# Performance work log

Hardware: AMD Instinct MI355X
Metric: run time of the kernel (lower is better)

## Reference

```python
import jax, jax.numpy as jnp
import numpy as np

B, C, H, W = 8, 256, 64, 64
CQK = C // 8  # 32


def setup_inputs() -> dict:
    key = jax.random.key(0)
    ks = jax.random.split(key, 8)
    s = 0.05
    return {
        "x": jax.random.normal(ks[0], (B, C, H, W), dtype=jnp.float32),
        "wq": jax.random.normal(ks[1], (CQK, C), dtype=jnp.float32) * s,
        "bq": jax.random.normal(ks[2], (CQK,), dtype=jnp.float32) * s,
        "wk": jax.random.normal(ks[3], (CQK, C), dtype=jnp.float32) * s,
        "bk": jax.random.normal(ks[4], (CQK,), dtype=jnp.float32) * s,
        "wv": jax.random.normal(ks[5], (C, C), dtype=jnp.float32) * s,
        "bv": jax.random.normal(ks[6], (C,), dtype=jnp.float32) * s,
        "gamma": jax.random.normal(ks[7], (1,), dtype=jnp.float32),
    }


def reference(x, wq, bq, wk, bk, wv, bv, gamma):
    b, c, h, w = x.shape
    xf = x.reshape(b, c, h * w)  # [B, C, N]
    # conv1d kernel-size-1 == per-token linear over channels
    f = jnp.einsum('oc,bcn->bon', wq, xf) + bq[None, :, None]  # [B, C/8, N]
    g = jnp.einsum('oc,bcn->bon', wk, xf) + bk[None, :, None]  # [B, C/8, N]
    hh = jnp.einsum('oc,bcn->bon', wv, xf) + bv[None, :, None]  # [B, C, N]
    # scores[b, i, j] = sum_o f[b, o, i] * g[b, o, j]; NO 1/sqrt(d) scaling
    scores = jnp.einsum('boi,boj->bij', f, g)  # [B, N, N]
    # softmax over dim=1 (the f/query index axis), as in the original
    beta = jax.nn.softmax(scores, axis=1)
    # o[b, c, j] = gamma * sum_i hh[b, c, i] * beta[b, i, j] + xf
    o = gamma[0] * jnp.einsum('bci,bij->bcj', hh, beta) + xf
    return o.reshape(b, c, h, w)
```

## Files before the change

### kernel.cpp

```cpp
#include <hip/hip_runtime.h>
#include <stdint.h>

#define B_ 8
#define C_ 256
#define N_ 4096
#define LOG2E 1.44269504088896f
#define NSHIFT_L2E (-14.0f * 1.44269504088896f)

typedef _Float16 half8 __attribute__((ext_vector_type(8)));
typedef _Float16 half4 __attribute__((ext_vector_type(4)));
typedef float floatx4 __attribute__((ext_vector_type(4)));

__global__ __launch_bounds__(256) void k_wprep(const float* __restrict__ wq, const float* __restrict__ bq,
                                               const float* __restrict__ wk, const float* __restrict__ bk,
                                               const float* __restrict__ wv, const float* __restrict__ bv,
                                               _Float16* __restrict__ Whf, float* __restrict__ Bh) {
    int r = blockIdx.x;
    int t = threadIdx.x;
    const float* src;
    float bias;
    if (r < 32)      { src = wq + r * 256;        bias = bq[r]; }
    else if (r < 64) { src = wk + (r - 32) * 256; bias = bk[r - 32]; }
    else             { src = wv + (r - 64) * 256; bias = bv[r - 64]; }
    Whf[(t >> 3) * 2560 + r * 8 + (t & 7)] = (_Float16)src[t];
    if (t == 0) Bh[r] = bias;
}

__global__ __launch_bounds__(256) void k_proj(const float* __restrict__ x,
                                              const _Float16* __restrict__ Whf,
                                              const float* __restrict__ Bh,
                                              _Float16* __restrict__ Kf,
                                              _Float16* __restrict__ Qf,
                                              _Float16* __restrict__ Vf) {
    __shared__ float xtile[64 * 65];
    __shared__ _Float16 As[64 * 264] __attribute__((aligned(16)));
    int id = blockIdx.x;
    int b  = id & 7;
    int i0 = (id >> 3) * 64;
    int t = threadIdx.x;
    int w = t >> 6, lane = t & 63, col = lane & 15, q = lane >> 4;
    const float* xb = x + (size_t)b * C_ * N_ + i0;
    for (int cc = 0; cc < 4; ++cc) {
        int cr = t >> 4;
        int ip = (t & 15) * 4;
#pragma unroll
        for (int k = 0; k < 4; ++k)
            *(float4*)&xtile[(cr + 16 * k) * 65 + ip] =
                *(const float4*)&xb[(size_t)(cc * 64 + cr + 16 * k) * N_ + ip];
        __syncthreads();
        int i = t & 63, cb2 = (t >> 6) * 16;
        float v[16];
#pragma unroll
        for (int k = 0; k < 16; ++k) v[k] = xtile[(cb2 + k) * 65 + i];
        half8 h0, h1;
#pragma unroll
        for (int k = 0; k < 8; ++k) { h0[k] = (_Float16)v[k]; h1[k] = (_Float16)v[8 + k]; }
        *(half8*)&As[i * 264 + cc * 64 + cb2] = h0;
        *(half8*)&As[i * 264 + cc * 64 + cb2 + 8] = h1;
        __syncthreads();
    }
    floatx4 acc[4][5];
#pragma unroll
    for (int mt = 0; mt < 4; ++mt)
#pragma unroll
        for (int nt = 0; nt < 5; ++nt) acc[mt][nt] = (floatx4){0.f, 0.f, 0.f, 0.f};
    for (int kc = 0; kc < 8; ++kc) {
        half8 a[4], bf[5];
#pragma unroll
        for (int nt = 0; nt < 5; ++nt)
            bf[nt] = *(const half8*)&Whf[(kc * 4 + q) * 2560 + (w * 80 + nt * 16 + col) * 8];
#pragma unroll
        for (int mt = 0; mt < 4; ++mt)
            a[mt] = *(const half8*)&As[(mt * 16 + col) * 264 + kc * 32 + q * 8];
#pragma unroll
        for (int mt = 0; mt < 4; ++mt)
#pragma unroll
            for (int nt = 0; nt < 5; ++nt)
                acc[mt][nt] = __builtin_amdgcn_mfma_f32_16x16x32_f16(a[mt], bf[nt], acc[mt][nt], 0, 0, 0);
    }
#pragma unroll
    for (int nt = 0; nt < 5; ++nt) {
        int n = w * 80 + nt * 16 + col;
        float bias = Bh[n];
        if (n < 32) {
#pragma unroll
            for (int mt = 0; mt < 4; ++mt)
#pragma unroll
                for (int r = 0; r < 4; ++r) {
                    int i = i0 + mt * 16 + q * 4 + r;
                    Kf[((((size_t)b * 128 + (i >> 5)) * 4 + (n >> 3)) * 32 + (i & 31)) * 8 + (n & 7)]
                        = (_Float16)(acc[mt][nt][r] + bias);
                }
        } else if (n < 64) {
            int n2 = n - 32;
#pragma unroll
            for (int mt = 0; mt < 4; ++mt)
#pragma unroll
                for (int r = 0; r < 4; ++r) {
                    int j = i0 + mt * 16 + q * 4 + r;
                    Qf[((((size_t)b * 128 + (j >> 5)) * 4 + (n2 >> 3)) * 32 + (j & 31)) * 8 + (n2 & 7)]
                        = (_Float16)(acc[mt][nt][r] + bias);
                }
        } else {
            int c = n - 64;
#pragma unroll
            for (int mt = 0; mt < 4; ++mt) {
                int ib = (i0 >> 4) + mt;
                half4 v4;
#pragma unroll
                for (int r = 0; r < 4; ++r) v4[r] = (_Float16)(acc[mt][nt][r] + bias);
                *(half4*)&Vf[(((size_t)b * 256 + ib) * 256 + c) * 16 + q * 4] = v4;
            }
        }
    }
}

#define PS_BUF 4608

#define ATTN_STEP(IT, VCUR, VNXT, ROFF, WOFF)                                     \
    {                                                                             \
        if ((IT) < 63) {                                                          \
            _Pragma("unroll")                                                     \
            for (int ct = 0; ct < 2; ++ct) {                                      \
                VNXT[ct * 2 + 0] = *(const half8*)(pV0 + ct * 256);               \
                VNXT[ct * 2 + 1] = *(const half8*)(pV1 + ct * 256);               \
            }                                                                     \
            pV0 += 16384; pV1 += 16384;                                           \
            aKn0 = *(const half8*)(pK);                                           \
            aKn1 = *(const half8*)(pK + 128);                                     \
            pK += 2048;                                                           \
        }                                                                         \
        _Pragma("unroll")                                                         \
        for (int kk = 0; kk < 2; ++kk) {                                          \
            half8 bfr[4];                                                         \
            _Pragma("unroll")                                                     \
            for (int jt = 0; jt < 4; ++jt)                                        \
                bfr[jt] = *(const half8*)&PsF[psr + (ROFF) + jt * 1152 + kk * 32];\
            _Pragma("unroll")                                                     \
            for (int ct = 0; ct < 2; ++ct)                                        \
                _Pragma("unroll")                                                 \
                for (int jt = 0; jt < 4; ++jt)                                    \
                    acc[ct][jt] = __builtin_amdgcn_mfma_f32_16x16x32_f16(         \
                        VCUR[ct * 2 + kk], bfr[jt], acc[ct][jt], 0, 0, 0);        \
        }                                                                         \
        if ((IT) < 63) {                                                          \
            _Pragma("unroll")                                                     \
            for (int itl = 0; itl < 2; ++itl) {                                   \
                floatx4 s = __builtin_amdgcn_mfma_f32_16x16x32_f16(               \
                    itl ? aKn1 : aKn0, bq, (floatx4){0.f, 0.f, 0.f, 0.f}, 0, 0, 0);\
                float p0 = exp2f(s[0] * LOG2E + NSHIFT_L2E);                      \
                float p1 = exp2f(s[1] * LOG2E + NSHIFT_L2E);                      \
                float p2 = exp2f(s[2] * LOG2E + NSHIFT_L2E);                      \
                float p3 = exp2f(s[3] * LOG2E + NSHIFT_L2E);                      \
                lacc += (p0 + p1) + (p2 + p3);                                    \
                half4 ph;                                                         \
                ph[0] = (_Float16)p0; ph[1] = (_Float16)p1;                       \
                ph[2] = (_Float16)p2; ph[3] = (_Float16)p3;                       \
                *(half4*)&PsF[psw + (WOFF) + itl * 16] = ph;                      \
            }                                                                     \
        }                                                                         \
        __syncthreads();                                                          \
    }

__global__ __launch_bounds__(512, 4) void k_attn(const _Float16* __restrict__ Kf,
                                                 const _Float16* __restrict__ Qf,
                                                 const _Float16* __restrict__ Vf,
                                                 const float* __restrict__ x,
                                                 const float* __restrict__ gptr,
                                                 float* __restrict__ out) {
    __shared__ _Float16 PsF[2 * PS_BUF] __attribute__((aligned(16)));
    __shared__ float Lp[2][64];
    int id = blockIdx.x;
    int b  = id & 7;
    int j0 = (id >> 3) * 64;
    int t = threadIdx.x;
    int w = t >> 6, lane = t & 63, col = lane & 15, q = lane >> 4;
    int jts = w & 3, ihs = w >> 2;
    int cw  = w * 32;
    const _Float16* Kfb = Kf + (size_t)b * 131072;
    const _Float16* Qfb = Qf + (size_t)b * 131072;
    const _Float16* Vfb = Vf + (size_t)b * 1048576;
    const _Float16* pK  = Kfb + ((ihs * 4 + q) * 32 + col) * 8;
    const _Float16* pV0 = Vfb + ((q >> 1) * 256 + cw + col) * 16 + (q & 1) * 8;
    const _Float16* pV1 = pV0 + 8192;
    const int psw = (jts * 16 + col) * 72 + ihs * 32 + q * 4;
    const int psr = col * 72 + q * 8;
    floatx4 acc[2][4];
#pragma unroll
    for (int ct = 0; ct < 2; ++ct)
#pragma unroll
        for (int jt = 0; jt < 4; ++jt) acc[ct][jt] = (floatx4){0.f, 0.f, 0.f, 0.f};
    float lacc = 0.f;
    half8 vA[4], vB[4], aKn0, aKn1;
#pragma unroll
    for (int ct = 0; ct < 2; ++ct) {
        vA[ct * 2 + 0] = *(const half8*)(pV0 + ct * 256);
        vA[ct * 2 + 1] = *(const half8*)(pV1 + ct * 256);
    }
    pV0 += 16384; pV1 += 16384;
    aKn0 = *(const half8*)(pK);
    aKn1 = *(const half8*)(pK + 128);
    pK += 2048;
    int jj = j0 + jts * 16;
    half8 bq = *(const half8*)&Qfb[(((jj >> 5) * 4 + q) * 32 + ((jj & 31) + col)) * 8];
#pragma unroll
    for (int itl = 0; itl < 2; ++itl) {
        floatx4 s = __builtin_amdgcn_mfma_f32_16x16x32_f16(itl ? aKn1 : aKn0, bq,
                                                           (floatx4){0.f, 0.f, 0.f, 0.f}, 0, 0, 0);
        float p0 = exp2f(s[0] * LOG2E + NSHIFT_L2E);
        float p1 = exp2f(s[1] * LOG2E + NSHIFT_L2E);
        float p2 = exp2f(s[2] * LOG2E + NSHIFT_L2E);
        float p3 = exp2f(s[3] * LOG2E + NSHIFT_L2E);
        lacc += (p0 + p1) + (p2 + p3);
        half4 ph;
        ph[0] = (_Float16)p0; ph[1] = (_Float16)p1;
        ph[2] = (_Float16)p2; ph[3] = (_Float16)p3;
        *(half4*)&PsF[psw + itl * 16] = ph;
    }
    __syncthreads();
    for (int m = 0; m < 32; ++m) {
        int it = m * 2;
        ATTN_STEP(it,     vA, vB, 0,      PS_BUF)
        ATTN_STEP(it + 1, vB, vA, PS_BUF, 0)
    }
    lacc += __shfl_xor(lacc, 16, 64);
    lacc += __shfl_xor(lacc, 32, 64);
    if (lane < 16) Lp[ihs][jts * 16 + lane] = lacc;
    __syncthreads();
    float gamma = gptr[0];
    const float* xb = x + (size_t)b * C_ * N_;
    float* ob = out + (size_t)b * C_ * N_;
#pragma unroll
    for (int jt = 0; jt < 4; ++jt) {
        int jl = jt * 16 + col;
        float li = 1.0f / (Lp[0][jl] + Lp[1][jl]);
        int j = j0 + jl;
#pragma unroll
        for (int ct = 0; ct < 2; ++ct)
#pragma unroll
            for (int r = 0; r < 4; ++r) {
                int c = cw + ct * 16 + q * 4 + r;
                size_t off = (size_t)c * N_ + j;
                ob[off] = gamma * acc[ct][jt][r] * li + xb[off];
            }
    }
}

extern "C" void kernel_launch(void* const* d_in, const int* in_sizes, int n_in,
                              void* d_out, int out_size, void* d_ws, size_t ws_size,
                              hipStream_t stream) {
    const float* x  = (const float*)d_in[0];
    const float* wq = (const float*)d_in[1];
    const float* bq = (const float*)d_in[2];
    const float* wk = (const float*)d_in[3];
    const float* bk = (const float*)d_in[4];
    const float* wv = (const float*)d_in[5];
    const float* bv = (const float*)d_in[6];
    const float* gm = (const float*)d_in[7];
    float* out = (float*)d_out;
    char* ws = (char*)d_ws;
    _Float16* Vf  = (_Float16*)ws;
    _Float16* Kf  = (_Float16*)(ws + 16777216);
    _Float16* Qf  = (_Float16*)(ws + 18874368);
    _Float16* Whf = (_Float16*)(ws + 20971520);
    float*    Bh  = (float*)(ws + 21135360);

    k_wprep<<<dim3(320), 256, 0, stream>>>(wq, bq, wk, bk, wv, bv, Whf, Bh);
    k_proj<<<dim3(512), 256, 0, stream>>>(x, Whf, Bh, Kf, Qf, Vf);
    k_attn<<<dim3(512), 512, 0, stream>>>(Kf, Qf, Vf, x, gm, out);
}
```

Baseline: 192.6 us.

## Fold log2e into K projection, swizzle P smem, pack-convert and lighten barrier

The K projection output is pre-scaled by log2e, and the softmax shift is passed as the MFMA accumulator init. This removes a per-element FMA before each exp2. The P tile in shared memory drops its padded stride for an XOR-swizzled layout that avoids bank conflicts, and fp16 conversion uses packed round-toward-zero conversions. __syncthreads is replaced by an explicit lgkmcnt wait plus s_barrier, so outstanding global loads no longer stall the barrier. Round-toward-zero conversion and the fp16 rounding of the prescaled K slightly change numerics.

```diff
diff --git a/kernel.cpp b/kernel.cpp
--- a/kernel.cpp
+++ b/kernel.cpp
@@ -9,6 +9,7 @@
 
 typedef _Float16 half8 __attribute__((ext_vector_type(8)));
 typedef _Float16 half4 __attribute__((ext_vector_type(4)));
+typedef __fp16  fp16x2 __attribute__((ext_vector_type(2)));
 typedef float floatx4 __attribute__((ext_vector_type(4)));
 
 __global__ __launch_bounds__(256) void k_wprep(const float* __restrict__ wq, const float* __restrict__ bq,
@@ -89,7 +90,7 @@
                 for (int r = 0; r < 4; ++r) {
                     int i = i0 + mt * 16 + q * 4 + r;
                     Kf[((((size_t)b * 128 + (i >> 5)) * 4 + (n >> 3)) * 32 + (i & 31)) * 8 + (n & 7)]
-                        = (_Float16)(acc[mt][nt][r] + bias);
+                        = (_Float16)((acc[mt][nt][r] + bias) * LOG2E);
                 }
         } else if (n < 64) {
             int n2 = n - 32;
@@ -115,7 +116,7 @@
     }
 }
 
-#define PS_BUF 4608
+#define PS_BUF 4096
 
 #define ATTN_STEP(IT, VCUR, VNXT, ROFF, WOFF)                                     \
     {                                                                             \
@@ -135,7 +136,7 @@
             half8 bfr[4];                                                         \
             _Pragma("unroll")                                                     \
             for (int jt = 0; jt < 4; ++jt)                                        \
-                bfr[jt] = *(const half8*)&PsF[psr + (ROFF) + jt * 1152 + kk * 32];\
+                bfr[jt] = *(const half8*)&PsF[(ROFF) + jt * 1024 + (kk ? ro1 : ro0)]; \
             _Pragma("unroll")                                                     \
             for (int ct = 0; ct < 2; ++ct)                                        \
                 _Pragma("unroll")                                                 \
@@ -147,19 +148,20 @@
             _Pragma("unroll")                                                     \
             for (int itl = 0; itl < 2; ++itl) {                                   \
                 floatx4 s = __builtin_amdgcn_mfma_f32_16x16x32_f16(               \
-                    itl ? aKn1 : aKn0, bq, (floatx4){0.f, 0.f, 0.f, 0.f}, 0, 0, 0);\
-                float p0 = exp2f(s[0] * LOG2E + NSHIFT_L2E);                      \
-                float p1 = exp2f(s[1] * LOG2E + NSHIFT_L2E);                      \
-                float p2 = exp2f(s[2] * LOG2E + NSHIFT_L2E);                      \
-                float p3 = exp2f(s[3] * LOG2E + NSHIFT_L2E);                      \
+                    itl ? aKn1 : aKn0, bq, cns, 0, 0, 0);                         \
+                float p0 = exp2f(s[0]);                                           \
+                float p1 = exp2f(s[1]);                                           \
+                float p2 = exp2f(s[2]);                                           \
+                float p3 = exp2f(s[3]);                                           \
                 lacc += (p0 + p1) + (p2 + p3);                                    \
-                half4 ph;                                                         \
-                ph[0] = (_Float16)p0; ph[1] = (_Float16)p1;                       \
-                ph[2] = (_Float16)p2; ph[3] = (_Float16)p3;                       \
-                *(half4*)&PsF[psw + (WOFF) + itl * 16] = ph;                      \
+                union { fp16x2 v; uint32_t u; } plo, phi;                         \
+                plo.v = __builtin_amdgcn_cvt_pkrtz(p0, p1);                       \
+                phi.v = __builtin_amdgcn_cvt_pkrtz(p2, p3);                       \
+                uint2 pw; pw.x = plo.u; pw.y = phi.u;                             \
+                *(uint2*)&PsF[(WOFF) + (itl ? wo1 : wo0)] = pw;                   \
             }                                                                     \
         }                                                                         \
-        __syncthreads();                                                          \
+        asm volatile("s_waitcnt lgkmcnt(0)\n\ts_barrier" ::: "memory");           \
     }
 
 __global__ __launch_bounds__(512, 4) void k_attn(const _Float16* __restrict__ Kf,
@@ -183,8 +185,12 @@
     const _Float16* pK  = Kfb + ((ihs * 4 + q) * 32 + col) * 8;
     const _Float16* pV0 = Vfb + ((q >> 1) * 256 + cw + col) * 16 + (q & 1) * 8;
     const _Float16* pV1 = pV0 + 8192;
-    const int psw = (jts * 16 + col) * 72 + ihs * 32 + q * 4;
-    const int psr = col * 72 + q * 8;
+    const int cswz = col & 7;
+    const int ro0 = col * 64 + ((q ^ cswz) << 3);
+    const int ro1 = ro0 ^ 32;
+    const int wo0 = (jts * 16 + col) * 64 + (((ihs << 2) ^ (q >> 1) ^ cswz) << 3) + (q & 1) * 4;
+    const int wo1 = wo0 ^ 16;
+    const floatx4 cns = {NSHIFT_L2E, NSHIFT_L2E, NSHIFT_L2E, NSHIFT_L2E};
     floatx4 acc[2][4];
 #pragma unroll
     for (int ct = 0; ct < 2; ++ct)
@@ -205,19 +211,19 @@
     half8 bq = *(const half8*)&Qfb[(((jj >> 5) * 4 + q) * 32 + ((jj & 31) + col)) * 8];
 #pragma unroll
     for (int itl = 0; itl < 2; ++itl) {
-        floatx4 s = __builtin_amdgcn_mfma_f32_16x16x32_f16(itl ? aKn1 : aKn0, bq,
-                                                           (floatx4){0.f, 0.f, 0.f, 0.f}, 0, 0, 0);
-        float p0 = exp2f(s[0] * LOG2E + NSHIFT_L2E);
-        float p1 = exp2f(s[1] * LOG2E + NSHIFT_L2E);
-        float p2 = exp2f(s[2] * LOG2E + NSHIFT_L2E);
-        float p3 = exp2f(s[3] * LOG2E + NSHIFT_L2E);
+        floatx4 s = __builtin_amdgcn_mfma_f32_16x16x32_f16(itl ? aKn1 : aKn0, bq, cns, 0, 0, 0);
+        float p0 = exp2f(s[0]);
+        float p1 = exp2f(s[1]);
+        float p2 = exp2f(s[2]);
+        float p3 = exp2f(s[3]);
         lacc += (p0 + p1) + (p2 + p3);
-        half4 ph;
-        ph[0] = (_Float16)p0; ph[1] = (_Float16)p1;
-        ph[2] = (_Float16)p2; ph[3] = (_Float16)p3;
-        *(half4*)&PsF[psw + itl * 16] = ph;
-    }
-    __syncthreads();
+        union { fp16x2 v; uint32_t u; } plo, phi;
+        plo.v = __builtin_amdgcn_cvt_pkrtz(p0, p1);
+        phi.v = __builtin_amdgcn_cvt_pkrtz(p2, p3);
+        uint2 pw; pw.x = plo.u; pw.y = phi.u;
+        *(uint2*)&PsF[itl ? wo1 : wo0] = pw;
+    }
+    asm volatile("s_waitcnt lgkmcnt(0)\n\ts_barrier" ::: "memory");
     for (int m = 0; m < 32; ++m) {
         int it = m * 2;
         ATTN_STEP(it,     vA, vB, 0,      PS_BUF)
```

Measured after the change: 190.2 us. About the same (-1.3%).
